# Optimization experiments

Measured on AMD Instinct MI355X. Metric: run time of the kernel, lower is better.

The kernel has to match this reference:

```python
import jax, jax.numpy as jnp
import numpy as np

N_HEADS = 8
D_K = 64
NEG = 1e9


def setup_inputs() -> dict:
    key = jax.random.key(0)
    k1, k2, k3 = jax.random.split(key, 3)
    B, L, C = 4, 2048, 512
    x = jax.random.normal(k1, (B, L, C), dtype=jnp.float32)
    W_in = jax.random.normal(k2, (C, N_HEADS * D_K * 3), dtype=jnp.float32) * (C ** -0.5)
    b_in = jnp.zeros((N_HEADS * D_K * 3,), dtype=jnp.float32)
    W_out = jax.random.normal(k3, (N_HEADS * D_K, C), dtype=jnp.float32) * ((N_HEADS * D_K) ** -0.5)
    b_out = jnp.zeros((C,), dtype=jnp.float32)
    return {"x": x, "W_in": W_in, "b_in": b_in, "W_out": W_out, "b_out": b_out}


def reference(x, W_in, b_in, W_out, b_out):
    B, L, C = x.shape
    H, Dk = N_HEADS, D_K
    scale = Dk ** -0.5
    qkv = x @ W_in + b_in                       # [B, L, 3*H*Dk]
    qkv = qkv.reshape(B, L, H, 3 * Dk)
    q, k, v = jnp.split(qkv, 3, axis=-1)         # each [B, L, H, Dk]
    attn = jnp.einsum('bihd,bjhd->bijh', q, k) * scale  # [B, L, L, H]
    mask = jnp.tril(jnp.ones((L, L), dtype=x.dtype))[None, :, :, None]
    attn = attn * mask - NEG * (1.0 - mask)
    attn = jax.nn.softmax(attn, axis=2)          # softmax over j
    res = jnp.einsum('bijh,bjhd->bihd', attn, v)  # [B, L, H, Dk]
    res = res.reshape(B, L, H * Dk)
    res = res @ W_out + b_out
    return res + x
```

## Files before the change

kernel.cpp:

```cpp
#include <hip/hip_runtime.h>
#include <hip/hip_bf16.h>
#include <math.h>
#include <cstddef>
#include <cstring>


constexpr int B_SZ  = 4;
constexpr int L_SEQ = 2048;
constexpr int C_DIM = 512;
constexpr int H_N   = 8;
constexpr int DK    = 64;
constexpr int N_QKV = 1536;
constexpr int M_ROWS = B_SZ * L_SEQ;
constexpr float QSCALE = 0.125f * 1.44269504088896f;
constexpr float DEFER_THR = 11.5f;

typedef __attribute__((ext_vector_type(4))) float f32x4;
typedef __attribute__((ext_vector_type(8))) short bf16x8;

static __device__ inline ushort f2bf(float f) {
  unsigned u = __builtin_bit_cast(unsigned, f);
  u += 0x7fffu + ((u >> 16) & 1u);
  return (ushort)(u >> 16);
}

static __device__ inline unsigned pack_bf2(float a, float b) {
  const __hip_bfloat162 v = __float22bfloat162_rn(make_float2(a, b));
  unsigned u;
  __builtin_memcpy(&u, &v, 4);
  return u;
}

typedef __attribute__((address_space(1))) const unsigned int* gas1_t;
typedef __attribute__((address_space(3))) unsigned int* las3_t;
static __device__ inline void gload_lds16(const void* g, void* l) {
  __builtin_amdgcn_global_load_lds((gas1_t)g, (las3_t)l, 16, 0, 0);
}


__global__ __launch_bounds__(256) void convert_bf16(
    const float* __restrict__ src, ushort* __restrict__ dst, int n4) {
  const int i = blockIdx.x * 256 + threadIdx.x;
  if (i < n4) {
    const float4 v = reinterpret_cast<const float4*>(src)[i];
    ushort4 o;
    o.x = f2bf(v.x); o.y = f2bf(v.y); o.z = f2bf(v.z); o.w = f2bf(v.w);
    reinterpret_cast<ushort4*>(dst)[i] = o;
  }
}

__global__ __launch_bounds__(256) void transpose_bf16(
    const float* __restrict__ src, ushort* __restrict__ dst, int R, int C) {
  __shared__ ushort T[64][65];
  const int c0 = blockIdx.x * 64, r0 = blockIdx.y * 64;
#pragma unroll
  for (int p = 0; p < 16; ++p) {
    const int idx = threadIdx.x + p * 256;
    const int r = idx >> 6, c = idx & 63;
    T[r][c] = f2bf(src[(size_t)(r0 + r) * C + c0 + c]);
  }
  __syncthreads();
#pragma unroll
  for (int p = 0; p < 16; ++p) {
    const int idx = threadIdx.x + p * 256;
    const int r = idx >> 6, c = idx & 63;
    dst[(size_t)(c0 + r) * R + r0 + c] = T[c][r];
  }
}

template <int EPI>
__global__ __launch_bounds__(256) void gemm_bf16(
    const ushort* __restrict__ A, const ushort* __restrict__ Bt,
    const float* __restrict__ bias, ushort* __restrict__ Qo,
    ushort* __restrict__ Ko, ushort* __restrict__ Vto,
    float* __restrict__ outF, const float* __restrict__ resid,
    int N, int K) {
  __shared__ ushort Al[128 * 32];
  __shared__ ushort Bl[128 * 32];
  const int tid = threadIdx.x;
  const int w = tid >> 6, l = tid & 63;
  const int cc = l & 15, gg = l >> 4;
  const int bm = blockIdx.y * 128, bn = blockIdx.x * 128;
  const int wr = w >> 1, wc = w & 1;
  f32x4 acc[4][4] = {};

  for (int k0 = 0; k0 < K; k0 += 32) {
#pragma unroll
    for (int q = 0; q < 2; ++q) {
      const int cbase = q * 256 + w * 64;
      const int c = cbase + l;
      gload_lds16(A + (size_t)(bm + (c >> 2)) * K + k0 + (c & 3) * 8,
                  &Al[cbase * 8]);
      gload_lds16(Bt + (size_t)(bn + (c >> 2)) * K + k0 + (c & 3) * 8,
                  &Bl[cbase * 8]);
    }
    __syncthreads();
    bf16x8 aF[4], bF[4];
#pragma unroll
    for (int i = 0; i < 4; ++i)
      aF[i] = *reinterpret_cast<const bf16x8*>(
          &Al[(wr * 64 + i * 16 + cc) * 32 + gg * 8]);
#pragma unroll
    for (int j = 0; j < 4; ++j)
      bF[j] = *reinterpret_cast<const bf16x8*>(
          &Bl[(wc * 64 + j * 16 + cc) * 32 + gg * 8]);
#pragma unroll
    for (int i = 0; i < 4; ++i)
#pragma unroll
      for (int j = 0; j < 4; ++j)
        acc[i][j] = __builtin_amdgcn_mfma_f32_16x16x32_bf16(aF[i], bF[j],
                                                            acc[i][j], 0, 0, 0);
    __syncthreads();
  }

  if (EPI == 0) {
#pragma unroll
    for (int j = 0; j < 4; ++j) {
      const int colbase = bn + wc * 64 + j * 16;
      const int h = colbase / 192, rem = colbase % 192;
      const int type = rem / 64, d = (rem % 64) + cc;
      const float bv = bias[colbase + cc];
#pragma unroll
      for (int i = 0; i < 4; ++i) {
        const int rowbase = bm + wr * 64 + i * 16 + 4 * gg;
        const int b = rowbase >> 11, ll = rowbase & 2047;
        const size_t bh32 = (size_t)(b * H_N + h) * 32;
        if (type == 0) {
#pragma unroll
          for (int r = 0; r < 4; ++r)
            Qo[((size_t)(b * H_N + h) * L_SEQ + ll + r) * DK + d] =
                f2bf((acc[i][j][r] + bv) * QSCALE);
        } else if (type == 1) {
#pragma unroll
          for (int r = 0; r < 4; ++r) {
            const int jg = ll + r;
            Ko[(bh32 + (jg >> 6)) * 4096 + (jg & 63) * 64 +
               (((d >> 3) ^ (jg & 7)) << 3) + (d & 7)] =
                f2bf(acc[i][j][r] + bv);
          }
        } else {
#pragma unroll
          for (int r = 0; r < 4; ++r) {
            const int jj = (ll & 63) + r;
            const int p = 4 * (jj & 15) + (jj >> 4);
            const int phys = (((p >> 3) ^ (d & 7)) << 3) | (p & 7);
            Vto[(bh32 + (ll >> 6)) * 4096 + (size_t)d * 64 + phys] =
                f2bf(acc[i][j][r] + bv);
          }
        }
      }
    }
  } else {
#pragma unroll
    for (int j = 0; j < 4; ++j) {
      const int col = bn + wc * 64 + j * 16 + cc;
      const float bv = bias[col];
#pragma unroll
      for (int i = 0; i < 4; ++i) {
        const int rowbase = bm + wr * 64 + i * 16 + 4 * gg;
#pragma unroll
        for (int r = 0; r < 4; ++r) {
          const size_t off = (size_t)(rowbase + r) * N + col;
          outF[off] = acc[i][j][r] + bv + resid[off];
        }
      }
    }
  }
}

#define STAGE(buf, tile)                                                     \
  {                                                                          \
    const ushort* kg_ = KoB + (size_t)(tile) * 4096 + w * 1024 + lane * 8;   \
    const ushort* vg_ = VtB + (size_t)(tile) * 4096 + w * 1024 + lane * 8;   \
    gload_lds16(kg_, &Ks[buf][w * 1024]);                                    \
    gload_lds16(kg_ + 512, &Ks[buf][w * 1024 + 512]);                        \
    gload_lds16(vg_, &Vs[buf][w * 1024]);                                    \
    gload_lds16(vg_ + 512, &Vs[buf][w * 1024 + 512]);                        \
  }

__global__ __launch_bounds__(256, 4) void attn_mfma(
    const ushort* __restrict__ Q, const ushort* __restrict__ Ko,
    const ushort* __restrict__ Vt, ushort* __restrict__ attn_out) {
  __shared__ ushort Ks[2][4096];
  __shared__ ushort Vs[2][4096];
  __shared__ ushort Pw_s[4][1024];
  const int id = blockIdx.x;
  const int bh = (id & 7) + 8 * ((id >> 3) & 3);
  const int qt = 31 - (id >> 5);
  const int tid = threadIdx.x;
  const int w = tid >> 6, lane = tid & 63;
  const int c = lane & 15, g = lane >> 4;
  const int b = bh >> 3, h = bh & 7;
  const ushort* KoB = Ko + (size_t)bh * 32 * 4096;
  const ushort* VtB = Vt + (size_t)bh * 32 * 4096;
  const int q0 = qt * 64 + w * 16;
  ushort* Pw = Pw_s[w];
  const int pc0 = (g ^ (c & 7)) * 8;
  const int pc1 = ((g + 4) ^ (c & 7)) * 8;

  bf16x8 qA[2];
  {
    const ushort* qp = Q + ((size_t)bh * L_SEQ + q0 + c) * DK + g * 8;
    qA[0] = *reinterpret_cast<const bf16x8*>(qp);
    qA[1] = *reinterpret_cast<const bf16x8*>(qp + 32);
  }

  f32x4 O[4] = {};
  float mrow[4] = {-INFINITY, -INFINITY, -INFINITY, -INFINITY};
  float lsum[4] = {};
  const f32x4 zero4 = {0.f, 0.f, 0.f, 0.f};

  STAGE(0, 0);
  __syncthreads();

  for (int jt = 0; jt <= qt; ++jt) {
    const int cur = jt & 1;
    if (jt < qt) STAGE(cur ^ 1, jt + 1);
    const ushort* Kc = Ks[cur];
    const ushort* Vc = Vs[cur];
    const int j0 = jt * 64;
    f32x4 S[4];
#pragma unroll
    for (int n = 0; n < 4; ++n) {
      const bf16x8 k0 = *reinterpret_cast<const bf16x8*>(&Kc[(n * 16 + c) * 64 + pc0]);
      const bf16x8 k1 = *reinterpret_cast<const bf16x8*>(&Kc[(n * 16 + c) * 64 + pc1]);
      S[n] = __builtin_amdgcn_mfma_f32_16x16x32_bf16(qA[0], k0, zero4, 0, 0, 0);
      S[n] = __builtin_amdgcn_mfma_f32_16x16x32_bf16(qA[1], k1, S[n], 0, 0, 0);
    }
    if (jt == qt) {
#pragma unroll
      for (int n = 0; n < 4; ++n)
#pragma unroll
        for (int r = 0; r < 4; ++r)
          if ((j0 + n * 16 + c) > (q0 + 4 * g + r)) S[n][r] = -INFINITY;
    }
    float pm[4];
    int exceed = 0;
#pragma unroll
    for (int r = 0; r < 4; ++r) {
      pm[r] = fmaxf(fmaxf(S[0][r], S[1][r]), fmaxf(S[2][r], S[3][r]));
      exceed |= (pm[r] > mrow[r] + DEFER_THR);
    }
    if (__any(exceed)) {
#pragma unroll
      for (int r = 0; r < 4; ++r) {
        float fm = pm[r];
        fm = fmaxf(fm, __shfl_xor(fm, 1, 16));
        fm = fmaxf(fm, __shfl_xor(fm, 2, 16));
        fm = fmaxf(fm, __shfl_xor(fm, 4, 16));
        fm = fmaxf(fm, __shfl_xor(fm, 8, 16));
        const float mnew = fmaxf(mrow[r], fm);
        const float corr = __builtin_exp2f(mrow[r] - mnew);
        lsum[r] *= corr;
#pragma unroll
        for (int t = 0; t < 4; ++t) O[t][r] *= corr;
        mrow[r] = mnew;
      }
    }
#pragma unroll
    for (int n = 0; n < 4; ++n)
#pragma unroll
      for (int r = 0; r < 4; ++r) {
        const float p = __builtin_exp2f(S[n][r] - mrow[r]);
        S[n][r] = p;
        lsum[r] += p;
      }
#pragma unroll
    for (int r = 0; r < 4; ++r) {
      const int row = 4 * g + r;
      uint2 pk2;
      pk2.x = pack_bf2(S[0][r], S[1][r]);
      pk2.y = pack_bf2(S[2][r], S[3][r]);
      *reinterpret_cast<uint2*>(
          &Pw[row * 64 + (((c >> 1) ^ (row & 7)) << 3) + 4 * (c & 1)]) = pk2;
    }
    const bf16x8 pA0 = *reinterpret_cast<const bf16x8*>(&Pw[c * 64 + pc0]);
    const bf16x8 pA1 = *reinterpret_cast<const bf16x8*>(&Pw[c * 64 + pc1]);
#pragma unroll
    for (int t = 0; t < 4; ++t) {
      const bf16x8 v0 = *reinterpret_cast<const bf16x8*>(&Vc[(t * 16 + c) * 64 + pc0]);
      const bf16x8 v1 = *reinterpret_cast<const bf16x8*>(&Vc[(t * 16 + c) * 64 + pc1]);
      O[t] = __builtin_amdgcn_mfma_f32_16x16x32_bf16(pA0, v0, O[t], 0, 0, 0);
      O[t] = __builtin_amdgcn_mfma_f32_16x16x32_bf16(pA1, v1, O[t], 0, 0, 0);
    }
    __syncthreads();
  }
  float inv[4];
#pragma unroll
  for (int r = 0; r < 4; ++r) {
    float s = lsum[r];
    s += __shfl_xor(s, 1, 16);
    s += __shfl_xor(s, 2, 16);
    s += __shfl_xor(s, 4, 16);
    s += __shfl_xor(s, 8, 16);
    inv[r] = 1.f / s;
  }
#pragma unroll
  for (int t = 0; t < 4; ++t)
#pragma unroll
    for (int r = 0; r < 4; ++r)
      attn_out[((size_t)b * L_SEQ + q0 + 4 * g + r) * C_DIM + h * DK + t * 16 + c] =
          f2bf(O[t][r] * inv[r]);
}

extern "C" void kernel_launch(void* const* d_in, const int* in_sizes, int n_in,
                              void* d_out, int out_size, void* d_ws,
                              size_t ws_size, hipStream_t stream) {
  const float* x     = (const float*)d_in[0];
  const float* W_in  = (const float*)d_in[1];
  const float* b_in  = (const float*)d_in[2];
  const float* W_out = (const float*)d_in[3];
  const float* b_out = (const float*)d_in[4];
  float* out = (float*)d_out;

  ushort* xbf   = (ushort*)d_ws;
  ushort* WinT  = xbf + (size_t)M_ROWS * C_DIM;
  ushort* WoutT = WinT + (size_t)N_QKV * C_DIM;
  ushort* Qo    = WoutT + (size_t)C_DIM * C_DIM;
  ushort* Ko    = Qo + (size_t)M_ROWS * C_DIM;
  ushort* Vto   = Ko + (size_t)M_ROWS * C_DIM;
  ushort* attnb = Vto + (size_t)M_ROWS * C_DIM;

  convert_bf16<<<(M_ROWS * C_DIM / 4 + 255) / 256, 256, 0, stream>>>(
      x, xbf, M_ROWS * C_DIM / 4);
  transpose_bf16<<<dim3(N_QKV / 64, C_DIM / 64), 256, 0, stream>>>(
      W_in, WinT, C_DIM, N_QKV);
  transpose_bf16<<<dim3(C_DIM / 64, C_DIM / 64), 256, 0, stream>>>(
      W_out, WoutT, C_DIM, C_DIM);

  gemm_bf16<0><<<dim3(N_QKV / 128, M_ROWS / 128), 256, 0, stream>>>(
      xbf, WinT, b_in, Qo, Ko, Vto, nullptr, nullptr, N_QKV, C_DIM);
  attn_mfma<<<dim3(1024, 1, 1), 256, 0, stream>>>(Qo, Ko, Vto, attnb);
  gemm_bf16<1><<<dim3(C_DIM / 128, M_ROWS / 128), 256, 0, stream>>>(
      attnb, WoutT, b_out, nullptr, nullptr, nullptr, out, x, C_DIM, C_DIM);
}
```

Before: 106.2 us.

## Pair causal query tiles per block and repack V/P layouts for vectorized stores

Each attention block now handles a pair of query tiles (qt and 31-qt), so every block does the same total causal work. The grid is halved to 512 blocks and launch bounds are relaxed from 4 to 2 blocks per SM. The V-transposed layout written by the QKV GEMM changes so four consecutive rows go out as one 8-byte store. The P tile is now written to LDS as scalar ushort stores in a new layout. The aim is to remove tail imbalance from the causal triangle and cut uncoalesced V scatter, at the cost of fewer resident blocks and more scalar LDS writes for P.

```diff
diff --git a/kernel.cpp b/kernel.cpp
--- a/kernel.cpp
+++ b/kernel.cpp
@@ -139,14 +139,14 @@
                 f2bf(acc[i][j][r] + bv);
           }
         } else {
-#pragma unroll
-          for (int r = 0; r < 4; ++r) {
-            const int jj = (ll & 63) + r;
-            const int p = 4 * (jj & 15) + (jj >> 4);
-            const int phys = (((p >> 3) ^ (d & 7)) << 3) | (p & 7);
-            Vto[(bh32 + (ll >> 6)) * 4096 + (size_t)d * 64 + phys] =
-                f2bf(acc[i][j][r] + bv);
-          }
+          ushort4 pk;
+          pk.x = f2bf(acc[i][j][0] + bv);
+          pk.y = f2bf(acc[i][j][1] + bv);
+          pk.z = f2bf(acc[i][j][2] + bv);
+          pk.w = f2bf(acc[i][j][3] + bv);
+          const size_t idx = (bh32 + (ll >> 6)) * 4096 + (size_t)d * 64 +
+                             ((((ll & 63) >> 3) ^ (d & 7)) << 3) + (ll & 7);
+          *reinterpret_cast<ushort4*>(&Vto[idx]) = pk;
         }
       }
     }
@@ -178,7 +178,7 @@
     gload_lds16(vg_ + 512, &Vs[buf][w * 1024 + 512]);                        \
   }
 
-__global__ __launch_bounds__(256, 4) void attn_mfma(
+__global__ __launch_bounds__(256, 2) void attn_mfma(
     const ushort* __restrict__ Q, const ushort* __restrict__ Ko,
     const ushort* __restrict__ Vt, ushort* __restrict__ attn_out) {
   __shared__ ushort Ks[2][4096];
@@ -186,121 +186,127 @@
   __shared__ ushort Pw_s[4][1024];
   const int id = blockIdx.x;
   const int bh = (id & 7) + 8 * ((id >> 3) & 3);
-  const int qt = 31 - (id >> 5);
+  const int pair = (id >> 5) & 15;
   const int tid = threadIdx.x;
   const int w = tid >> 6, lane = tid & 63;
   const int c = lane & 15, g = lane >> 4;
   const int b = bh >> 3, h = bh & 7;
   const ushort* KoB = Ko + (size_t)bh * 32 * 4096;
   const ushort* VtB = Vt + (size_t)bh * 32 * 4096;
-  const int q0 = qt * 64 + w * 16;
   ushort* Pw = Pw_s[w];
   const int pc0 = (g ^ (c & 7)) * 8;
   const int pc1 = ((g + 4) ^ (c & 7)) * 8;
-
-  bf16x8 qA[2];
-  {
-    const ushort* qp = Q + ((size_t)bh * L_SEQ + q0 + c) * DK + g * 8;
-    qA[0] = *reinterpret_cast<const bf16x8*>(qp);
-    qA[1] = *reinterpret_cast<const bf16x8*>(qp + 32);
-  }
-
-  f32x4 O[4] = {};
-  float mrow[4] = {-INFINITY, -INFINITY, -INFINITY, -INFINITY};
-  float lsum[4] = {};
   const f32x4 zero4 = {0.f, 0.f, 0.f, 0.f};
 
-  STAGE(0, 0);
-  __syncthreads();
-
-  for (int jt = 0; jt <= qt; ++jt) {
-    const int cur = jt & 1;
-    if (jt < qt) STAGE(cur ^ 1, jt + 1);
-    const ushort* Kc = Ks[cur];
-    const ushort* Vc = Vs[cur];
-    const int j0 = jt * 64;
-    f32x4 S[4];
-#pragma unroll
-    for (int n = 0; n < 4; ++n) {
-      const bf16x8 k0 = *reinterpret_cast<const bf16x8*>(&Kc[(n * 16 + c) * 64 + pc0]);
-      const bf16x8 k1 = *reinterpret_cast<const bf16x8*>(&Kc[(n * 16 + c) * 64 + pc1]);
-      S[n] = __builtin_amdgcn_mfma_f32_16x16x32_bf16(qA[0], k0, zero4, 0, 0, 0);
-      S[n] = __builtin_amdgcn_mfma_f32_16x16x32_bf16(qA[1], k1, S[n], 0, 0, 0);
-    }
-    if (jt == qt) {
+  for (int ps = 0; ps < 2; ++ps) {
+    const int qt = ps ? pair : (31 - pair);
+    const int q0 = qt * 64 + w * 16;
+
+    bf16x8 qA[2];
+    {
+      const ushort* qp = Q + ((size_t)bh * L_SEQ + q0 + c) * DK + g * 8;
+      qA[0] = *reinterpret_cast<const bf16x8*>(qp);
+      qA[1] = *reinterpret_cast<const bf16x8*>(qp + 32);
+    }
+    f32x4 O[4] = {};
+    float mrow[4] = {-INFINITY, -INFINITY, -INFINITY, -INFINITY};
+    float lsum[4] = {};
+
+    STAGE(0, 0);
+    __syncthreads();
+
+    for (int jt = 0; jt <= qt; ++jt) {
+      const int cur = jt & 1;
+      if (jt < qt) STAGE(cur ^ 1, jt + 1);
+      const ushort* Kc = Ks[cur];
+      const ushort* Vc = Vs[cur];
+      f32x4 S[4];
+#pragma unroll
+      for (int n = 0; n < 4; ++n) {
+        const bf16x8 k0 = *reinterpret_cast<const bf16x8*>(&Kc[(n * 16 + c) * 64 + pc0]);
+        const bf16x8 k1 = *reinterpret_cast<const bf16x8*>(&Kc[(n * 16 + c) * 64 + pc1]);
+        S[n] = __builtin_amdgcn_mfma_f32_16x16x32_bf16(qA[0], k0, zero4, 0, 0, 0);
+        S[n] = __builtin_amdgcn_mfma_f32_16x16x32_bf16(qA[1], k1, S[n], 0, 0, 0);
+      }
+      if (jt == qt) {
+        const int j0 = jt * 64;
+#pragma unroll
+        for (int n = 0; n < 4; ++n)
+#pragma unroll
+          for (int r = 0; r < 4; ++r)
+            if ((j0 + n * 16 + c) > (q0 + 4 * g + r)) S[n][r] = -INFINITY;
+      }
+      float pm[4];
+      int exceed = 0;
+#pragma unroll
+      for (int r = 0; r < 4; ++r) {
+        pm[r] = fmaxf(fmaxf(S[0][r], S[1][r]), fmaxf(S[2][r], S[3][r]));
+        exceed |= (pm[r] > mrow[r] + DEFER_THR);
+      }
+      if (__any(exceed)) {
+#pragma unroll
+        for (int r = 0; r < 4; ++r) {
+          float fm = pm[r];
+          fm = fmaxf(fm, __shfl_xor(fm, 1, 16));
+          fm = fmaxf(fm, __shfl_xor(fm, 2, 16));
+          fm = fmaxf(fm, __shfl_xor(fm, 4, 16));
+          fm = fmaxf(fm, __shfl_xor(fm, 8, 16));
+          const float mnew = fmaxf(mrow[r], fm);
+          const float corr = __builtin_exp2f(mrow[r] - mnew);
+          lsum[r] *= corr;
+#pragma unroll
+          for (int t = 0; t < 4; ++t) O[t][r] *= corr;
+          mrow[r] = mnew;
+        }
+      }
 #pragma unroll
       for (int n = 0; n < 4; ++n)
 #pragma unroll
-        for (int r = 0; r < 4; ++r)
-          if ((j0 + n * 16 + c) > (q0 + 4 * g + r)) S[n][r] = -INFINITY;
-    }
-    float pm[4];
-    int exceed = 0;
+        for (int r = 0; r < 4; ++r) {
+          const float p = __builtin_exp2f(S[n][r] - mrow[r]);
+          S[n][r] = p;
+          lsum[r] += p;
+        }
+#pragma unroll
+      for (int n = 0; n < 4; ++n)
+#pragma unroll
+        for (int r = 0; r < 4; r += 2) {
+          const unsigned pk = pack_bf2(S[n][r], S[n][r + 1]);
+          const int row0 = 4 * g + r, row1 = row0 + 1;
+          Pw[row0 * 64 + ((2 * n + (c >> 3)) ^ (row0 & 7)) * 8 + (c & 7)] =
+              (ushort)(pk & 0xffffu);
+          Pw[row1 * 64 + ((2 * n + (c >> 3)) ^ (row1 & 7)) * 8 + (c & 7)] =
+              (ushort)(pk >> 16);
+        }
+      const bf16x8 pA0 = *reinterpret_cast<const bf16x8*>(&Pw[c * 64 + pc0]);
+      const bf16x8 pA1 = *reinterpret_cast<const bf16x8*>(&Pw[c * 64 + pc1]);
+#pragma unroll
+      for (int t = 0; t < 4; ++t) {
+        const bf16x8 v0 = *reinterpret_cast<const bf16x8*>(&Vc[(t * 16 + c) * 64 + pc0]);
+        const bf16x8 v1 = *reinterpret_cast<const bf16x8*>(&Vc[(t * 16 + c) * 64 + pc1]);
+        O[t] = __builtin_amdgcn_mfma_f32_16x16x32_bf16(pA0, v0, O[t], 0, 0, 0);
+        O[t] = __builtin_amdgcn_mfma_f32_16x16x32_bf16(pA1, v1, O[t], 0, 0, 0);
+      }
+      __syncthreads();
+    }
+    float inv[4];
 #pragma unroll
     for (int r = 0; r < 4; ++r) {
-      pm[r] = fmaxf(fmaxf(S[0][r], S[1][r]), fmaxf(S[2][r], S[3][r]));
-      exceed |= (pm[r] > mrow[r] + DEFER_THR);
-    }
-    if (__any(exceed)) {
-#pragma unroll
-      for (int r = 0; r < 4; ++r) {
-        float fm = pm[r];
-        fm = fmaxf(fm, __shfl_xor(fm, 1, 16));
-        fm = fmaxf(fm, __shfl_xor(fm, 2, 16));
-        fm = fmaxf(fm, __shfl_xor(fm, 4, 16));
-        fm = fmaxf(fm, __shfl_xor(fm, 8, 16));
-        const float mnew = fmaxf(mrow[r], fm);
-        const float corr = __builtin_exp2f(mrow[r] - mnew);
-        lsum[r] *= corr;
-#pragma unroll
-        for (int t = 0; t < 4; ++t) O[t][r] *= corr;
-        mrow[r] = mnew;
-      }
-    }
-#pragma unroll
-    for (int n = 0; n < 4; ++n)
-#pragma unroll
-      for (int r = 0; r < 4; ++r) {
-        const float p = __builtin_exp2f(S[n][r] - mrow[r]);
-        S[n][r] = p;
-        lsum[r] += p;
-      }
-#pragma unroll
-    for (int r = 0; r < 4; ++r) {
-      const int row = 4 * g + r;
-      uint2 pk2;
-      pk2.x = pack_bf2(S[0][r], S[1][r]);
-      pk2.y = pack_bf2(S[2][r], S[3][r]);
-      *reinterpret_cast<uint2*>(
-          &Pw[row * 64 + (((c >> 1) ^ (row & 7)) << 3) + 4 * (c & 1)]) = pk2;
-    }
-    const bf16x8 pA0 = *reinterpret_cast<const bf16x8*>(&Pw[c * 64 + pc0]);
-    const bf16x8 pA1 = *reinterpret_cast<const bf16x8*>(&Pw[c * 64 + pc1]);
-#pragma unroll
-    for (int t = 0; t < 4; ++t) {
-      const bf16x8 v0 = *reinterpret_cast<const bf16x8*>(&Vc[(t * 16 + c) * 64 + pc0]);
-      const bf16x8 v1 = *reinterpret_cast<const bf16x8*>(&Vc[(t * 16 + c) * 64 + pc1]);
-      O[t] = __builtin_amdgcn_mfma_f32_16x16x32_bf16(pA0, v0, O[t], 0, 0, 0);
-      O[t] = __builtin_amdgcn_mfma_f32_16x16x32_bf16(pA1, v1, O[t], 0, 0, 0);
-    }
+      float s = lsum[r];
+      s += __shfl_xor(s, 1, 16);
+      s += __shfl_xor(s, 2, 16);
+      s += __shfl_xor(s, 4, 16);
+      s += __shfl_xor(s, 8, 16);
+      inv[r] = 1.f / s;
+    }
+#pragma unroll
+    for (int t = 0; t < 4; ++t)
+#pragma unroll
+      for (int r = 0; r < 4; ++r)
+        attn_out[((size_t)b * L_SEQ + q0 + 4 * g + r) * C_DIM + h * DK + t * 16 + c] =
+            f2bf(O[t][r] * inv[r]);
     __syncthreads();
   }
-  float inv[4];
-#pragma unroll
-  for (int r = 0; r < 4; ++r) {
-    float s = lsum[r];
-    s += __shfl_xor(s, 1, 16);
-    s += __shfl_xor(s, 2, 16);
-    s += __shfl_xor(s, 4, 16);
-    s += __shfl_xor(s, 8, 16);
-    inv[r] = 1.f / s;
-  }
-#pragma unroll
-  for (int t = 0; t < 4; ++t)
-#pragma unroll
-    for (int r = 0; r < 4; ++r)
-      attn_out[((size_t)b * L_SEQ + q0 + 4 * g + r) * C_DIM + h * DK + t * 16 + c] =
-          f2bf(O[t][r] * inv[r]);
 }
 
 extern "C" void kernel_launch(void* const* d_in, const int* in_sizes, int n_in,
@@ -330,7 +336,7 @@
 
   gemm_bf16<0><<<dim3(N_QKV / 128, M_ROWS / 128), 256, 0, stream>>>(
       xbf, WinT, b_in, Qo, Ko, Vto, nullptr, nullptr, N_QKV, C_DIM);
-  attn_mfma<<<dim3(1024, 1, 1), 256, 0, stream>>>(Qo, Ko, Vto, attnb);
+  attn_mfma<<<dim3(512, 1, 1), 256, 0, stream>>>(Qo, Ko, Vto, attnb);
   gemm_bf16<1><<<dim3(C_DIM / 128, M_ROWS / 128), 256, 0, stream>>>(
       attnb, WoutT, b_out, nullptr, nullptr, nullptr, out, x, C_DIM, C_DIM);
 }
```

Result: no change. 104.5 us (-1.7%).
